# Optimization experiments

Hardware: AMD Instinct MI355X
Metric: run time of the kernel (lower is better)

Reference implementation:

```python
import jax, jax.numpy as jnp
import numpy as np

LN_EPS = 1e-5   # torch nn.LayerNorm default eps
L2_EPS = 1e-12  # torch F.normalize default eps


def setup_inputs() -> dict:
    key = jax.random.key(0)
    k1, k2 = jax.random.split(key)
    b, c, h, w = 4, 256, 128, 256
    num_classes, num_prototype, proj_dim = 19, 10, 256
    x = jax.random.normal(k1, (b, c, h, w), dtype=jnp.float32)
    # trunc_normal_(std=0.02) approximated by normal * 0.02 (l2-normalized in fwd anyway)
    prototypes = jax.random.normal(k2, (num_classes, num_prototype, proj_dim), dtype=jnp.float32) * 0.02
    mask_norm_weight = jnp.ones((num_classes,), dtype=jnp.float32)
    mask_norm_bias = jnp.zeros((num_classes,), dtype=jnp.float32)
    return {"x": x, "prototypes": prototypes,
            "mask_norm_weight": mask_norm_weight, "mask_norm_bias": mask_norm_bias}


def _layer_norm(y, w, b):
    mu = jnp.mean(y, axis=-1, keepdims=True)
    var = jnp.var(y, axis=-1, keepdims=True)
    return (y - mu) * jax.lax.rsqrt(var + LN_EPS) * w + b


def reference(x, prototypes, mask_norm_weight, mask_norm_bias):
    b, c, h, w = x.shape
    # self.prototypes.data.copy_(l2_normalize(self.prototypes)) -- normalize over feature dim
    protos = prototypes / (jnp.linalg.norm(prototypes, axis=-1, keepdims=True) + L2_EPS)
    # rearrange 'b c h w -> (b h w) c'
    xf = x.transpose(0, 2, 3, 1).reshape(-1, c)           # [n, d]
    # cosine similarity: einsum('nd,kmd->nmk') then permute -> [n, k(classes), m(protos)]
    sim_mat = jnp.einsum('nd,kmd->nkm', xf, protos)       # [n, cls, proto]
    out_seg = jnp.max(sim_mat, axis=2)                    # amax over prototypes -> [n, cls]
    out_seg = _layer_norm(out_seg, mask_norm_weight, mask_norm_bias)
    # rearrange '(b h w) c -> b c h w'
    return out_seg.reshape(b, h, w, -1).transpose(0, 3, 1, 2)
```

## Files before the change

kernel.cpp:

```cpp
#include <hip/hip_runtime.h>


#define CC_   256
#define HW_   32768
#define NPIX_ 131072
#define NCLS_ 19
#define MBLK_ 128
#define SIMST_ 194

typedef __attribute__((ext_vector_type(8)))  short bf16x8;
typedef __attribute__((ext_vector_type(16))) float f32x16;
typedef __attribute__((ext_vector_type(4)))  float f32x4;
typedef __attribute__((ext_vector_type(2)))  float f32x2;
typedef __attribute__((ext_vector_type(4)))  unsigned int u32x4;
typedef __attribute__((ext_vector_type(2)))  unsigned int u32x2;

__device__ __forceinline__ void gll16(const void* g, void* l) {
  __builtin_amdgcn_global_load_lds((__attribute__((address_space(1))) void*)(g),
                                   (__attribute__((address_space(3))) void*)(l), 16, 0, 0);
}

#define RAWBAR() do {                                          \
  __builtin_amdgcn_sched_barrier(0);                           \
  asm volatile("s_waitcnt lgkmcnt(0)" ::: "memory");           \
  __builtin_amdgcn_s_barrier();                                \
  asm volatile("" ::: "memory");                               \
  __builtin_amdgcn_sched_barrier(0);                           \
} while (0)

__global__ void prep_protos(const float* __restrict__ protos, char* __restrict__ Bp) {
  const int p = blockIdx.x;
  const int l = threadIdx.x;
  __shared__ float pn[256];
  float v[4] = {0.f, 0.f, 0.f, 0.f};
  float sq = 0.f;
  if (p < 190) {
    #pragma unroll
    for (int i = 0; i < 4; ++i) {
      v[i] = protos[p * 256 + l * 4 + i];
      sq += v[i] * v[i];
    }
  }
  #pragma unroll
  for (int off = 32; off > 0; off >>= 1) sq += __shfl_xor(sq, off, 64);
  const float scale = (p < 190) ? 1.0f / (sqrtf(sq) + 1e-12f) : 0.0f;
  #pragma unroll
  for (int i = 0; i < 4; ++i) pn[l * 4 + i] = v[i] * scale;
  __syncthreads();

  const int oct  = l >> 1;
  const int part = l & 1;
  unsigned int w[4];
  #pragma unroll
  for (int pr = 0; pr < 4; ++pr) {
    const float f0 = pn[oct * 8 + 2 * pr];
    const float f1 = pn[oct * 8 + 2 * pr + 1];
    const unsigned int u0 = __builtin_bit_cast(unsigned int, f0);
    const unsigned int u1 = __builtin_bit_cast(unsigned int, f1);
    if (part == 0) {
      w[pr] = (u1 & 0xFFFF0000u) | (u0 >> 16);
    } else {
      const float t0 = __builtin_bit_cast(float, u0 & 0xFFFF0000u);
      const float t1 = __builtin_bit_cast(float, u1 & 0xFFFF0000u);
      const unsigned int v0 = __builtin_bit_cast(unsigned int, f0 - t0);
      const unsigned int v1 = __builtin_bit_cast(unsigned int, f1 - t1);
      w[pr] = (v1 & 0xFFFF0000u) | (v0 >> 16);
    }
  }
  const int cc = oct >> 2, ks = (oct >> 1) & 1, ko = oct & 1;
  const int nt = p >> 5, cL = p & 31;
  const size_t a16 = (size_t)((((cc * 2 + ks) * 6 + nt) * 2 + part) * 64 + ko * 32 + cL);
  *(u32x4*)(Bp + a16 * 16) = (u32x4){w[0], w[1], w[2], w[3]};
}

__device__ __forceinline__ void stageA(char* Albase, const f32x2* aLd,
                                       int ksw, int kow, int sub, int mtw, int r15w) {
  #pragma unroll
  for (int e = 0; e < 2; ++e) {
    unsigned int wh[2], wl[2];
    #pragma unroll
    for (int q = 0; q < 2; ++q) {
      const float f0 = aLd[2 * q][e];
      const float f1 = aLd[2 * q + 1][e];
      const unsigned int u0 = __builtin_bit_cast(unsigned int, f0);
      const unsigned int u1 = __builtin_bit_cast(unsigned int, f1);
      wh[q] = (u1 & 0xFFFF0000u) | (u0 >> 16);
      const float t0 = __builtin_bit_cast(float, u0 & 0xFFFF0000u);
      const float t1 = __builtin_bit_cast(float, u1 & 0xFFFF0000u);
      const unsigned int v0 = __builtin_bit_cast(unsigned int, f0 - t0);
      const unsigned int v1 = __builtin_bit_cast(unsigned int, f1 - t1);
      wl[q] = (v1 & 0xFFFF0000u) | (v0 >> 16);
    }
    const int slotH = ((ksw * 2 + 0) * 4 + mtw) * 64 + kow * 32 + e * 16 + r15w;
    const int slotL = ((ksw * 2 + 1) * 4 + mtw) * 64 + kow * 32 + e * 16 + r15w;
    *(u32x2*)(Albase + slotH * 16 + sub * 8) = (u32x2){wh[0], wh[1]};
    *(u32x2*)(Albase + slotL * 16 + sub * 8) = (u32x2){wl[0], wl[1]};
  }
}

__launch_bounds__(512, 4)
__global__ void gemm_kernel(const float* __restrict__ x, const char* __restrict__ Bp,
                            const float* __restrict__ mw, const float* __restrict__ mb,
                            float* __restrict__ out) {
  __shared__ __align__(16) char smem[65536];
  char* Albase = smem;
  char* Blbase = smem + 16384;

  const int tid  = threadIdx.x;
  const int wave = tid >> 6;
  const int lane = tid & 63;
  const int n0   = blockIdx.x * MBLK_;
  const int b    = n0 >> 15;
  const int hw0  = n0 & (HW_ - 1);
  const float* xb = x + (size_t)b * CC_ * HW_ + hw0;

  const int ksw = wave >> 2, kow = (wave >> 1) & 1, sub = wave & 1;
  const int mtw = lane >> 4, r15w = lane & 15;
  const float* xA = xb + (size_t)(wave * 4) * HW_ + 2 * lane;

  const int rowg = wave >> 1, colg = wave & 1;

  f32x16 acc[3];
  #pragma unroll
  for (int nt = 0; nt < 3; ++nt) acc[nt] = (f32x16)(0.0f);

  f32x2 aLd[4];

  #pragma unroll
  for (int j = 0; j < 4; ++j) aLd[j] = *(const f32x2*)(xA + (size_t)j * HW_);
  #pragma unroll
  for (int i = 0; i < 3; ++i)
    gll16(Bp + (size_t)(tid + 512 * i) * 16, Blbase + (tid + 512 * i) * 16);
  stageA(Albase, aLd, ksw, kow, sub, mtw, r15w);
  __syncthreads();

  #pragma unroll
  for (int cc = 0; cc < 8; ++cc) {
    const int buf = cc & 1;
    if (cc < 7) {
      const float* xn = xA + (size_t)((cc + 1) * 32) * HW_;
      #pragma unroll
      for (int j = 0; j < 4; ++j) aLd[j] = *(const f32x2*)(xn + (size_t)j * HW_);
      #pragma unroll
      for (int i = 0; i < 3; ++i)
        gll16(Bp + (size_t)((cc + 1) * 1536 + tid + 512 * i) * 16,
              Blbase + (buf ^ 1) * 24576 + (tid + 512 * i) * 16);
    }
    const char* Bq = Blbase + buf * 24576;
    #pragma unroll
    for (int ks = 0; ks < 2; ++ks) {
      const bf16x8 ah = *(const bf16x8*)(Albase + (size_t)((((ks * 2 + 0) * 4 + rowg) * 64 + lane) * 16));
      const bf16x8 al = *(const bf16x8*)(Albase + (size_t)((((ks * 2 + 1) * 4 + rowg) * 64 + lane) * 16));
      #pragma unroll
      for (int nt = 0; nt < 3; ++nt) {
        const int ntg = colg * 3 + nt;
        const bf16x8 bh = *(const bf16x8*)(Bq + (size_t)(((ks * 12 + ntg * 2 + 0) * 64 + lane) * 16));
        const bf16x8 bl = *(const bf16x8*)(Bq + (size_t)(((ks * 12 + ntg * 2 + 1) * 64 + lane) * 16));
        acc[nt] = __builtin_amdgcn_mfma_f32_32x32x16_bf16(ah, bh, acc[nt], 0, 0, 0);
        acc[nt] = __builtin_amdgcn_mfma_f32_32x32x16_bf16(al, bh, acc[nt], 0, 0, 0);
        acc[nt] = __builtin_amdgcn_mfma_f32_32x32x16_bf16(ah, bl, acc[nt], 0, 0, 0);
      }
    }
    RAWBAR();
    if (cc < 7) stageA(Albase, aLd, ksw, kow, sub, mtw, r15w);
    __syncthreads();
  }

  float* sims = (float*)smem;
  #pragma unroll 1
  for (int r = 0; r < 2; ++r) {
    if ((rowg >> 1) == r) {
      const int srow = (rowg & 1) * 32;
      #pragma unroll
      for (int nt = 0; nt < 3; ++nt) {
        #pragma unroll
        for (int q = 0; q < 16; ++q) {
          const int row = (q & 3) + 8 * (q >> 2) + 4 * (lane >> 5);
          sims[(srow + row) * SIMST_ + (colg * 3 + nt) * 32 + (lane & 31)] = acc[nt][q];
        }
      }
    }
    __syncthreads();
    if (tid < 64) {
      float mx[NCLS_];
      #pragma unroll
      for (int k = 0; k < NCLS_; ++k) {
        const float* rp = sims + tid * SIMST_ + k * 10;
        const f32x2 v0 = *(const f32x2*)(rp + 0);
        const f32x2 v1 = *(const f32x2*)(rp + 2);
        const f32x2 v2 = *(const f32x2*)(rp + 4);
        const f32x2 v3 = *(const f32x2*)(rp + 6);
        const f32x2 v4 = *(const f32x2*)(rp + 8);
        float m01 = fmaxf(fmaxf(v0[0], v0[1]), fmaxf(v1[0], v1[1]));
        float m23 = fmaxf(fmaxf(v2[0], v2[1]), fmaxf(v3[0], v3[1]));
        mx[k] = fmaxf(fmaxf(m01, m23), fmaxf(v4[0], v4[1]));
      }
      float mu = 0.f;
      #pragma unroll
      for (int k = 0; k < NCLS_; ++k) mu += mx[k];
      mu *= (1.0f / NCLS_);
      float var = 0.f;
      #pragma unroll
      for (int k = 0; k < NCLS_; ++k) { const float d = mx[k] - mu; var += d * d; }
      var *= (1.0f / NCLS_);
      const float rstd = rsqrtf(var + 1e-5f);
      const int s = tid & 31;
      const int hw = hw0 + (2 * r + (tid >> 5)) * 32 + ((s & 15) << 1) + (s >> 4);
      #pragma unroll
      for (int k = 0; k < NCLS_; ++k) {
        out[((size_t)(b * NCLS_ + k) << 15) + hw] = (mx[k] - mu) * rstd * mw[k] + mb[k];
      }
    }
    __syncthreads();
  }
}

extern "C" void kernel_launch(void* const* d_in, const int* in_sizes, int n_in,
                              void* d_out, int out_size, void* d_ws, size_t ws_size,
                              hipStream_t stream) {
  const float* x      = (const float*)d_in[0];
  const float* protos = (const float*)d_in[1];
  const float* mw     = (const float*)d_in[2];
  const float* mb     = (const float*)d_in[3];
  float* out = (float*)d_out;
  char* Bp   = (char*)d_ws;

  prep_protos<<<192, 64, 0, stream>>>(protos, Bp);
  gemm_kernel<<<NPIX_ / MBLK_, 512, 0, stream>>>(x, Bp, mw, mb, out);
}
```

Measured before the change: 204.1 us.

## Deepen global-load prefetch to two stages with explicit vmcnt-based barriers

Loads of x rows are now issued two K-chunks ahead into alternating register sets (aA/aB), and prototype tiles are prefetched two chunks ahead into the LDS buffer just consumed. The generic __syncthreads is replaced with barriers that wait on vmcnt(7) so that outstanding global loads can stay in flight across iterations. The aim is to hide HBM latency on the streaming x reads. In exchange it uses more registers, and the hand-counted vmcnt values must match the compiler's load ordering exactly or the kernel will race.

```diff
diff --git a/kernel.cpp b/kernel.cpp
--- a/kernel.cpp
+++ b/kernel.cpp
@@ -10,7 +10,6 @@
 
 typedef __attribute__((ext_vector_type(8)))  short bf16x8;
 typedef __attribute__((ext_vector_type(16))) float f32x16;
-typedef __attribute__((ext_vector_type(4)))  float f32x4;
 typedef __attribute__((ext_vector_type(2)))  float f32x2;
 typedef __attribute__((ext_vector_type(4)))  unsigned int u32x4;
 typedef __attribute__((ext_vector_type(2)))  unsigned int u32x2;
@@ -20,12 +19,18 @@
                                    (__attribute__((address_space(3))) void*)(l), 16, 0, 0);
 }
 
-#define RAWBAR() do {                                          \
-  __builtin_amdgcn_sched_barrier(0);                           \
-  asm volatile("s_waitcnt lgkmcnt(0)" ::: "memory");           \
-  __builtin_amdgcn_s_barrier();                                \
-  asm volatile("" ::: "memory");                               \
-  __builtin_amdgcn_sched_barrier(0);                           \
+#define SCHED() __builtin_amdgcn_sched_barrier(0)
+#define BAR_LG() do {                                            \
+  SCHED();                                                       \
+  asm volatile("s_waitcnt lgkmcnt(0)" ::: "memory");             \
+  __builtin_amdgcn_s_barrier();                                  \
+  SCHED();                                                       \
+} while (0)
+#define BAR_VMLG(N) do {                                         \
+  SCHED();                                                       \
+  asm volatile("s_waitcnt vmcnt(" #N ") lgkmcnt(0)" ::: "memory"); \
+  __builtin_amdgcn_s_barrier();                                  \
+  SCHED();                                                       \
 } while (0)
 
 __global__ void prep_protos(const float* __restrict__ protos, char* __restrict__ Bp) {
@@ -73,7 +78,7 @@
   *(u32x4*)(Bp + a16 * 16) = (u32x4){w[0], w[1], w[2], w[3]};
 }
 
-__device__ __forceinline__ void stageA(char* Albase, const f32x2* aLd,
+__device__ __forceinline__ void stageA(char* Albase, const f32x2 (&aLd)[4],
                                        int ksw, int kow, int sub, int mtw, int r15w) {
   #pragma unroll
   for (int e = 0; e < 2; ++e) {
@@ -124,27 +129,32 @@
   #pragma unroll
   for (int nt = 0; nt < 3; ++nt) acc[nt] = (f32x16)(0.0f);
 
-  f32x2 aLd[4];
-
-  #pragma unroll
-  for (int j = 0; j < 4; ++j) aLd[j] = *(const f32x2*)(xA + (size_t)j * HW_);
+  f32x2 aA[4], aB[4];
+
   #pragma unroll
   for (int i = 0; i < 3; ++i)
     gll16(Bp + (size_t)(tid + 512 * i) * 16, Blbase + (tid + 512 * i) * 16);
-  stageA(Albase, aLd, ksw, kow, sub, mtw, r15w);
-  __syncthreads();
+  SCHED();
+  #pragma unroll
+  for (int j = 0; j < 4; ++j) aA[j] = *(const f32x2*)(xA + (size_t)j * HW_);
+  SCHED();
+  #pragma unroll
+  for (int j = 0; j < 4; ++j) aB[j] = *(const f32x2*)(xA + (size_t)(32 + j) * HW_);
+  SCHED();
+  stageA(Albase, aA, ksw, kow, sub, mtw, r15w);
+  #pragma unroll
+  for (int i = 0; i < 3; ++i)
+    gll16(Bp + (size_t)(1536 + tid + 512 * i) * 16, Blbase + 24576 + (tid + 512 * i) * 16);
+  BAR_LG();
 
   #pragma unroll
   for (int cc = 0; cc < 8; ++cc) {
     const int buf = cc & 1;
-    if (cc < 7) {
-      const float* xn = xA + (size_t)((cc + 1) * 32) * HW_;
-      #pragma unroll
-      for (int j = 0; j < 4; ++j) aLd[j] = *(const f32x2*)(xn + (size_t)j * HW_);
-      #pragma unroll
-      for (int i = 0; i < 3; ++i)
-        gll16(Bp + (size_t)((cc + 1) * 1536 + tid + 512 * i) * 16,
-              Blbase + (buf ^ 1) * 24576 + (tid + 512 * i) * 16);
+    if (cc + 2 < 8) {
+      f32x2 (&dst)[4] = (cc & 1) ? aB : aA;
+      const float* xn = xA + (size_t)((cc + 2) * 32) * HW_;
+      #pragma unroll
+      for (int j = 0; j < 4; ++j) dst[j] = *(const f32x2*)(xn + (size_t)j * HW_);
     }
     const char* Bq = Blbase + buf * 24576;
     #pragma unroll
@@ -161,9 +171,19 @@
         acc[nt] = __builtin_amdgcn_mfma_f32_32x32x16_bf16(ah, bl, acc[nt], 0, 0, 0);
       }
     }
-    RAWBAR();
-    if (cc < 7) stageA(Albase, aLd, ksw, kow, sub, mtw, r15w);
-    __syncthreads();
+    BAR_LG();
+    if (cc + 2 < 8) {
+      #pragma unroll
+      for (int i = 0; i < 3; ++i)
+        gll16(Bp + (size_t)((cc + 2) * 1536 + tid + 512 * i) * 16,
+              Blbase + buf * 24576 + (tid + 512 * i) * 16);
+    }
+    if (cc < 7) {
+      f32x2 (&stg)[4] = (cc & 1) ? aA : aB;
+      stageA(Albase, stg, ksw, kow, sub, mtw, r15w);
+      if (cc < 6) BAR_VMLG(7);
+      else        BAR_VMLG(0);
+    }
   }
 
   float* sims = (float*)smem;
```

Measured after the change: 206.1 us. No clear change (+1.0%).
